# Performance work log

Hardware: AMD Instinct MI355X
Metric: run time of the kernel (lower is better)

## Reference

```python
import jax, jax.numpy as jnp
import numpy as np

B, N, C = 4, 4096, 32
S = 4096  # samples == N (square DFT matrix)


def setup_inputs() -> dict:
    key = jax.random.key(0)
    k1, k2 = jax.random.split(key)
    x = jax.random.normal(k1, (B, N, C), dtype=jnp.float32)
    t = jax.random.uniform(k2, (B, N), dtype=jnp.float32)  # sample times in [0,1]
    # learnable freqs initialized exactly as in the module: linspace(0,1,samples)
    freqs = jnp.linspace(0.0, 1.0, S).astype(jnp.float32)
    return {"x": x, "t": t, "freqs": freqs}


def reference(x, t, freqs):
    n = x.shape[1]
    # exponent_rows = -2*pi*i * (freqs*(n-1)) / n  -> purely imaginary, keep the real phase
    rows = (-2.0 * jnp.pi / n) * (freqs * (n - 1))          # [S]
    cols = t * (n - 1)                                       # [B, N]
    phase = rows[None, :, None] * cols[:, None, :]           # [B, S, N]
    fourier = jnp.exp(1j * phase.astype(jnp.complex64)) * (1.0 / np.sqrt(n)).astype(np.float32)
    z = jnp.einsum('bsn,bnc->bsc', fourier, x.astype(jnp.complex64))  # [B, S, C] complex
    # remove_zerocomp: zero first and last output rows
    z = z.at[:, 0].set(0).at[:, -1].set(0)
    # real=True -> magnitude as float32
    return jnp.abs(z).astype(jnp.float32)
```

## Files before the change

kernel.cpp:

```cpp
#include <hip/hip_runtime.h>
#include <hip/hip_fp16.h>
#include <math.h>

#define B_ 4
#define N_ 4096
#define C_ 32
#define S_ 4096
#define KW 512
#define NSTEP 16

typedef float f32x4 __attribute__((ext_vector_type(4)));
typedef _Float16 f16x8 __attribute__((ext_vector_type(8)));
typedef __fp16 fp16x2 __attribute__((ext_vector_type(2)));
typedef unsigned int uint_t;
typedef unsigned short ushort_t;

#define XTH_OFF 0
#define PSI_OFF (B_ * C_ * N_ * 2)
#define WS_NEED (PSI_OFF + B_ * N_ * 4)

__device__ __forceinline__ uint_t pkrtz(float a, float b) {
    union { fp16x2 h; uint_t w; } u;
    u.h = __builtin_amdgcn_cvt_pkrtz(a, b);
    return u.w;
}

__device__ __forceinline__ void sincos_ref(float p, float& sn, float& cs) {
    const double INV2PI_D = 0.15915494309189535;
    const float HI = (float)INV2PI_D;
    const float LO = (float)(INV2PI_D - (double)HI);
    float hi = p * HI;
    float e  = fmaf(p, HI, -hi);
    e = fmaf(p, LO, e);
    float k = rintf(hi);
    float r = (hi - k) + e;
    sn = __builtin_amdgcn_sinf(r);
    cs = __builtin_amdgcn_cosf(r);
}

__global__ __launch_bounds__(256)
void fudft_prep(const float* __restrict__ x, const float* __restrict__ t,
                ushort_t* __restrict__ xTh, float* __restrict__ psi)
{
    __shared__ ushort_t lds[64][40];
    const int tid = threadIdx.x;
    const int n0 = blockIdx.x * 64;
    const int b  = blockIdx.y;

    const float* src = x + ((size_t)b * N_ + n0) * C_;
    const int nl = tid >> 2, c0 = (tid & 3) * 8;
    const float4 v0 = *(const float4*)(src + (size_t)nl * C_ + c0);
    const float4 v1 = *(const float4*)(src + (size_t)nl * C_ + c0 + 4);
    const float vv[8] = {v0.x, v0.y, v0.z, v0.w, v1.x, v1.y, v1.z, v1.w};
    union { ushort_t u[8]; int4 i; } hp;
#pragma unroll
    for (int j = 0; j < 8; ++j) hp.u[j] = __half_as_ushort(__float2half_rn(vv[j]));
    *(int4*)&lds[nl][c0] = hp.i;

    if (tid < 64) psi[b * N_ + n0 + tid] = t[b * N_ + n0 + tid] * (float)(N_ - 1);
    __syncthreads();

    const int c = tid >> 3, oct = tid & 7;
    union { ushort_t u[8]; int4 i; } o;
#pragma unroll
    for (int j = 0; j < 8; ++j) o.u[j] = lds[oct * 8 + j][c];
    *(int4*)(xTh + ((size_t)(b * C_ + c)) * N_ + n0 + oct * 8) = o.i;
}

#define MFMA16(A, Bv, Acc) __builtin_amdgcn_mfma_f32_16x16x32_f16(A, Bv, Acc, 0, 0, 0)

__global__ __launch_bounds__(512, 4)
void fudft_mfma(const float* __restrict__ freqs,
                const ushort_t* __restrict__ xTh,
                const float* __restrict__ psi,
                float* __restrict__ out)
{
    __shared__ float red[14336];

    const int tid = threadIdx.x;
    const int wk = tid >> 6;
    const int lane = tid & 63;
    const int q = lane >> 4, r = lane & 15;
    const int b = blockIdx.y;
    const int sb = blockIdx.x * 32;

    const float rr0 = -(freqs[sb + r]      * (float)(N_ - 1)) * 0.000244140625f;
    const float rr1 = -(freqs[sb + 16 + r] * (float)(N_ - 1)) * 0.000244140625f;

    const float* pp = psi + (size_t)b * N_ + wk * KW + q * 8;
    const ushort_t* xb0 = xTh + ((size_t)(b * C_ + r)) * N_ + wk * KW + q * 8;
    const ushort_t* xb1 = xb0 + 16 * N_;

    f32x4 aRe0a = {0,0,0,0}, aIm0a = {0,0,0,0}, aRe0b = {0,0,0,0}, aIm0b = {0,0,0,0};
    f32x4 aRe1a = {0,0,0,0}, aIm1a = {0,0,0,0}, aRe1b = {0,0,0,0}, aIm1b = {0,0,0,0};

#pragma unroll
    for (int s = 0; s < NSTEP; ++s) {
        const float4 p0 = *(const float4*)(pp + s * 32);
        const float4 p1 = *(const float4*)(pp + s * 32 + 4);
        union { int4 i; f16x8 v; } b0, b1;
        b0.i = *(const int4*)(xb0 + s * 32);
        b1.i = *(const int4*)(xb1 + s * 32);

        const float ph[8] = {p0.x, p0.y, p0.z, p0.w, p1.x, p1.y, p1.z, p1.w};
        float c0v[8], s0v[8], c1v[8], s1v[8];
#pragma unroll
        for (int j = 0; j < 8; ++j) {
            float rv0 = __builtin_amdgcn_fractf(rr0 * ph[j]);
            s0v[j] = __builtin_amdgcn_sinf(rv0);
            c0v[j] = __builtin_amdgcn_cosf(rv0);
            float rv1 = __builtin_amdgcn_fractf(rr1 * ph[j]);
            s1v[j] = __builtin_amdgcn_sinf(rv1);
            c1v[j] = __builtin_amdgcn_cosf(rv1);
        }
        union { uint_t w[4]; f16x8 v; } fC0, fS0, fC1, fS1;
#pragma unroll
        for (int j = 0; j < 4; ++j) {
            fC0.w[j] = pkrtz(c0v[2*j], c0v[2*j+1]);
            fS0.w[j] = pkrtz(s0v[2*j], s0v[2*j+1]);
            fC1.w[j] = pkrtz(c1v[2*j], c1v[2*j+1]);
            fS1.w[j] = pkrtz(s1v[2*j], s1v[2*j+1]);
        }
        aRe0a = MFMA16(fC0.v, b0.v, aRe0a);  aRe0b = MFMA16(fC0.v, b1.v, aRe0b);
        aIm0a = MFMA16(fS0.v, b0.v, aIm0a);  aIm0b = MFMA16(fS0.v, b1.v, aIm0b);
        aRe1a = MFMA16(fC1.v, b0.v, aRe1a);  aRe1b = MFMA16(fC1.v, b1.v, aRe1b);
        aIm1a = MFMA16(fS1.v, b0.v, aIm1a);  aIm1b = MFMA16(fS1.v, b1.v, aIm1b);
    }

    if (wk > 0) {
        float* rb = red + (size_t)(wk - 1) * 8 * 256 + lane * 4;
        *(f32x4*)(rb + 0*256) = aRe0a;  *(f32x4*)(rb + 1*256) = aIm0a;
        *(f32x4*)(rb + 2*256) = aRe0b;  *(f32x4*)(rb + 3*256) = aIm0b;
        *(f32x4*)(rb + 4*256) = aRe1a;  *(f32x4*)(rb + 5*256) = aIm1a;
        *(f32x4*)(rb + 6*256) = aRe1b;  *(f32x4*)(rb + 7*256) = aIm1b;
    }
    __syncthreads();
    if (wk == 0) {
#pragma unroll
        for (int sl = 0; sl < 7; ++sl) {
            const float* rb = red + (size_t)sl * 8 * 256 + lane * 4;
            aRe0a += *(const f32x4*)(rb + 0*256);  aIm0a += *(const f32x4*)(rb + 1*256);
            aRe0b += *(const f32x4*)(rb + 2*256);  aIm0b += *(const f32x4*)(rb + 3*256);
            aRe1a += *(const f32x4*)(rb + 4*256);  aIm1a += *(const f32x4*)(rb + 5*256);
            aRe1b += *(const f32x4*)(rb + 6*256);  aIm1b += *(const f32x4*)(rb + 7*256);
        }
        float* po = out + ((size_t)b * S_ + sb) * C_;
#pragma unroll
        for (int reg = 0; reg < 4; ++reg) {
            const int m0 = q * 4 + reg, m1 = 16 + q * 4 + reg;
            const bool z0 = (sb + m0 == 0) || (sb + m0 == S_ - 1);
            const bool z1 = (sb + m1 == 0) || (sb + m1 == S_ - 1);
            float v;
            v = sqrtf(fmaf(aRe0a[reg], aRe0a[reg], aIm0a[reg]*aIm0a[reg])) * 0.015625f;
            po[(size_t)m0 * C_ + r]      = z0 ? 0.f : v;
            v = sqrtf(fmaf(aRe0b[reg], aRe0b[reg], aIm0b[reg]*aIm0b[reg])) * 0.015625f;
            po[(size_t)m0 * C_ + 16 + r] = z0 ? 0.f : v;
            v = sqrtf(fmaf(aRe1a[reg], aRe1a[reg], aIm1a[reg]*aIm1a[reg])) * 0.015625f;
            po[(size_t)m1 * C_ + r]      = z1 ? 0.f : v;
            v = sqrtf(fmaf(aRe1b[reg], aRe1b[reg], aIm1b[reg]*aIm1b[reg])) * 0.015625f;
            po[(size_t)m1 * C_ + 16 + r] = z1 ? 0.f : v;
        }
    }
}

__global__ __launch_bounds__(256)
void fudft_naive(const float* __restrict__ x, const float* __restrict__ t,
                 const float* __restrict__ freqs, float* __restrict__ out)
{
    const int s = blockIdx.x * 256 + threadIdx.x;
    const int b = blockIdx.y;
    const float row = (freqs[s] * (float)(N_ - 1)) * (float)(-2.0 * M_PI / (double)N_);
    float aR[C_], aI[C_];
#pragma unroll
    for (int c = 0; c < C_; ++c) { aR[c] = 0.f; aI[c] = 0.f; }
    for (int n = 0; n < N_; ++n) {
        const float col = t[b * N_ + n] * (float)(N_ - 1);
        float sn, cs; sincos_ref(row * col, sn, cs);
        const float* xr = x + ((size_t)b * N_ + n) * C_;
#pragma unroll
        for (int c = 0; c < C_; ++c) {
            aR[c] = fmaf(cs, xr[c], aR[c]);
            aI[c] = fmaf(sn, xr[c], aI[c]);
        }
    }
    float* dst = out + ((size_t)b * S_ + s) * C_;
    const bool zero = (s == 0) || (s == S_ - 1);
#pragma unroll
    for (int c = 0; c < C_; ++c) {
        const float m = sqrtf(fmaf(aR[c], aR[c], aI[c] * aI[c])) * 0.015625f;
        dst[c] = zero ? 0.f : m;
    }
}

extern "C" void kernel_launch(void* const* d_in, const int* in_sizes, int n_in,
                              void* d_out, int out_size, void* d_ws, size_t ws_size,
                              hipStream_t stream) {
    const float* x = (const float*)d_in[0];
    const float* t = (const float*)d_in[1];
    const float* f = (const float*)d_in[2];
    float* out = (float*)d_out;

    if (ws_size >= (size_t)WS_NEED) {
        char* ws = (char*)d_ws;
        ushort_t* xTh = (ushort_t*)(ws + XTH_OFF);
        float*    psi = (float*)(ws + PSI_OFF);

        dim3 gprep(N_ / 64, B_);
        fudft_prep<<<gprep, 256, 0, stream>>>(x, t, xTh, psi);
        dim3 grid(S_ / 32, B_);
        fudft_mfma<<<grid, 512, 0, stream>>>(f, xTh, psi, out);
    } else {
        dim3 grid(S_ / 256, B_);
        fudft_naive<<<grid, 256, 0, stream>>>(x, t, f, out);
    }
}
```

Measured before the change: 82.03 us.

## Split the N reduction across two blocks and add a reduce kernel

The MFMA kernel's reduction over N is split into two halves, one per grid slice. Each block writes complex partial sums to a workspace buffer, and a new reduce kernel adds the two halves and applies the magnitude and zeroing. This doubles the block count to 1024 with half the per-wave K work, targeting better occupancy and load balance. The in-block LDS reduction becomes a tree, with a smaller LDS footprint and a higher launch-bounds occupancy hint. In exchange it adds a kernel launch, an extra global round-trip of partials, and a larger workspace requirement, which could push execution onto the naive fallback if the workspace is too small.

```diff
diff --git a/kernel.cpp b/kernel.cpp
--- a/kernel.cpp
+++ b/kernel.cpp
@@ -6,8 +6,9 @@
 #define N_ 4096
 #define C_ 32
 #define S_ 4096
-#define KW 512
-#define NSTEP 16
+#define KB2 2048
+#define KW 256
+#define NSTEP 8
 
 typedef float f32x4 __attribute__((ext_vector_type(4)));
 typedef _Float16 f16x8 __attribute__((ext_vector_type(8)));
@@ -15,9 +16,11 @@
 typedef unsigned int uint_t;
 typedef unsigned short ushort_t;
 
-#define XTH_OFF 0
-#define PSI_OFF (B_ * C_ * N_ * 2)
-#define WS_NEED (PSI_OFF + B_ * N_ * 4)
+#define XTH_OFF  0
+#define PSI_OFF  (B_ * C_ * N_ * 2)
+#define PART_OFF (PSI_OFF + B_ * N_ * 4)
+#define PART_BYTES (B_ * 2 * S_ * 2 * C_ * 4)
+#define WS_NEED  (PART_OFF + PART_BYTES)
 
 __device__ __forceinline__ uint_t pkrtz(float a, float b) {
     union { fp16x2 h; uint_t w; } u;
@@ -69,26 +72,27 @@
 
 #define MFMA16(A, Bv, Acc) __builtin_amdgcn_mfma_f32_16x16x32_f16(A, Bv, Acc, 0, 0, 0)
 
-__global__ __launch_bounds__(512, 4)
+__global__ __launch_bounds__(512, 8)
 void fudft_mfma(const float* __restrict__ freqs,
                 const ushort_t* __restrict__ xTh,
                 const float* __restrict__ psi,
-                float* __restrict__ out)
-{
-    __shared__ float red[14336];
+                float* __restrict__ part)
+{
+    __shared__ float red[8192];
 
     const int tid = threadIdx.x;
     const int wk = tid >> 6;
     const int lane = tid & 63;
     const int q = lane >> 4, r = lane & 15;
-    const int b = blockIdx.y;
+    const int kh = blockIdx.y;
+    const int b = blockIdx.z;
     const int sb = blockIdx.x * 32;
 
     const float rr0 = -(freqs[sb + r]      * (float)(N_ - 1)) * 0.000244140625f;
     const float rr1 = -(freqs[sb + 16 + r] * (float)(N_ - 1)) * 0.000244140625f;
 
-    const float* pp = psi + (size_t)b * N_ + wk * KW + q * 8;
-    const ushort_t* xb0 = xTh + ((size_t)(b * C_ + r)) * N_ + wk * KW + q * 8;
+    const float* pp = psi + (size_t)b * N_ + kh * KB2 + wk * KW + q * 8;
+    const ushort_t* xb0 = xTh + ((size_t)(b * C_ + r)) * N_ + kh * KB2 + wk * KW + q * 8;
     const ushort_t* xb1 = xb0 + 16 * N_;
 
     f32x4 aRe0a = {0,0,0,0}, aIm0a = {0,0,0,0}, aRe0b = {0,0,0,0}, aIm0b = {0,0,0,0};
@@ -127,40 +131,60 @@
         aIm1a = MFMA16(fS1.v, b0.v, aIm1a);  aIm1b = MFMA16(fS1.v, b1.v, aIm1b);
     }
 
-    if (wk > 0) {
-        float* rb = red + (size_t)(wk - 1) * 8 * 256 + lane * 4;
+    auto store_slot = [&](int slot) {
+        float* rb = red + slot * 2048 + lane * 4;
         *(f32x4*)(rb + 0*256) = aRe0a;  *(f32x4*)(rb + 1*256) = aIm0a;
         *(f32x4*)(rb + 2*256) = aRe0b;  *(f32x4*)(rb + 3*256) = aIm0b;
         *(f32x4*)(rb + 4*256) = aRe1a;  *(f32x4*)(rb + 5*256) = aIm1a;
         *(f32x4*)(rb + 6*256) = aRe1b;  *(f32x4*)(rb + 7*256) = aIm1b;
-    }
+    };
+    auto add_slot = [&](int slot) {
+        const float* rb = red + slot * 2048 + lane * 4;
+        aRe0a += *(const f32x4*)(rb + 0*256);  aIm0a += *(const f32x4*)(rb + 1*256);
+        aRe0b += *(const f32x4*)(rb + 2*256);  aIm0b += *(const f32x4*)(rb + 3*256);
+        aRe1a += *(const f32x4*)(rb + 4*256);  aIm1a += *(const f32x4*)(rb + 5*256);
+        aRe1b += *(const f32x4*)(rb + 6*256);  aIm1b += *(const f32x4*)(rb + 7*256);
+    };
+
+    if (wk >= 4) store_slot(wk - 4);
+    __syncthreads();
+    if (wk < 4) add_slot(wk);
+    __syncthreads();
+    if (wk == 2 || wk == 3) store_slot(wk - 2);
+    __syncthreads();
+    if (wk < 2) add_slot(wk);
+    __syncthreads();
+    if (wk == 1) store_slot(0);
     __syncthreads();
     if (wk == 0) {
-#pragma unroll
-        for (int sl = 0; sl < 7; ++sl) {
-            const float* rb = red + (size_t)sl * 8 * 256 + lane * 4;
-            aRe0a += *(const f32x4*)(rb + 0*256);  aIm0a += *(const f32x4*)(rb + 1*256);
-            aRe0b += *(const f32x4*)(rb + 2*256);  aIm0b += *(const f32x4*)(rb + 3*256);
-            aRe1a += *(const f32x4*)(rb + 4*256);  aIm1a += *(const f32x4*)(rb + 5*256);
-            aRe1b += *(const f32x4*)(rb + 6*256);  aIm1b += *(const f32x4*)(rb + 7*256);
-        }
-        float* po = out + ((size_t)b * S_ + sb) * C_;
+        add_slot(0);
+        float* po = part + (((size_t)(b * 2 + kh) * S_ + sb) * C_) * 2;
 #pragma unroll
         for (int reg = 0; reg < 4; ++reg) {
             const int m0 = q * 4 + reg, m1 = 16 + q * 4 + reg;
-            const bool z0 = (sb + m0 == 0) || (sb + m0 == S_ - 1);
-            const bool z1 = (sb + m1 == 0) || (sb + m1 == S_ - 1);
-            float v;
-            v = sqrtf(fmaf(aRe0a[reg], aRe0a[reg], aIm0a[reg]*aIm0a[reg])) * 0.015625f;
-            po[(size_t)m0 * C_ + r]      = z0 ? 0.f : v;
-            v = sqrtf(fmaf(aRe0b[reg], aRe0b[reg], aIm0b[reg]*aIm0b[reg])) * 0.015625f;
-            po[(size_t)m0 * C_ + 16 + r] = z0 ? 0.f : v;
-            v = sqrtf(fmaf(aRe1a[reg], aRe1a[reg], aIm1a[reg]*aIm1a[reg])) * 0.015625f;
-            po[(size_t)m1 * C_ + r]      = z1 ? 0.f : v;
-            v = sqrtf(fmaf(aRe1b[reg], aRe1b[reg], aIm1b[reg]*aIm1b[reg])) * 0.015625f;
-            po[(size_t)m1 * C_ + 16 + r] = z1 ? 0.f : v;
-        }
-    }
+            *(float2*)(po + ((size_t)m0 * C_ + r) * 2)      = make_float2(aRe0a[reg], aIm0a[reg]);
+            *(float2*)(po + ((size_t)m0 * C_ + 16 + r) * 2) = make_float2(aRe0b[reg], aIm0b[reg]);
+            *(float2*)(po + ((size_t)m1 * C_ + r) * 2)      = make_float2(aRe1a[reg], aIm1a[reg]);
+            *(float2*)(po + ((size_t)m1 * C_ + 16 + r) * 2) = make_float2(aRe1b[reg], aIm1b[reg]);
+        }
+    }
+}
+
+__global__ __launch_bounds__(256)
+void fudft_reduce(const float* __restrict__ part, float* __restrict__ out)
+{
+    const int idx = blockIdx.x * 256 + threadIdx.x;
+    const int c2 = (idx & 15) * 2;
+    const int s = (idx >> 4) & (S_ - 1);
+    const int b = idx >> 16;
+    const float4 v0 = *(const float4*)(part + (((size_t)(b * 2 + 0) * S_ + s) * C_ + c2) * 2);
+    const float4 v1 = *(const float4*)(part + (((size_t)(b * 2 + 1) * S_ + s) * C_ + c2) * 2);
+    const float re0 = v0.x + v1.x, im0 = v0.y + v1.y;
+    const float re1 = v0.z + v1.z, im1 = v0.w + v1.w;
+    float m0 = sqrtf(fmaf(re0, re0, im0 * im0)) * 0.015625f;
+    float m1 = sqrtf(fmaf(re1, re1, im1 * im1)) * 0.015625f;
+    if (s == 0 || s == S_ - 1) { m0 = 0.f; m1 = 0.f; }
+    *(float2*)(out + ((size_t)b * S_ + s) * C_ + c2) = make_float2(m0, m1);
 }
 
 __global__ __launch_bounds__(256)
@@ -202,13 +226,15 @@
 
     if (ws_size >= (size_t)WS_NEED) {
         char* ws = (char*)d_ws;
-        ushort_t* xTh = (ushort_t*)(ws + XTH_OFF);
-        float*    psi = (float*)(ws + PSI_OFF);
+        ushort_t* xTh  = (ushort_t*)(ws + XTH_OFF);
+        float*    psi  = (float*)(ws + PSI_OFF);
+        float*    part = (float*)(ws + PART_OFF);
 
         dim3 gprep(N_ / 64, B_);
         fudft_prep<<<gprep, 256, 0, stream>>>(x, t, xTh, psi);
-        dim3 grid(S_ / 32, B_);
-        fudft_mfma<<<grid, 512, 0, stream>>>(f, xTh, psi, out);
+        dim3 grid(S_ / 32, 2, B_);
+        fudft_mfma<<<grid, 512, 0, stream>>>(f, xTh, psi, part);
+        fudft_reduce<<<(B_ * S_ * C_ / 2) / 256, 256, 0, stream>>>(part, out);
     } else {
         dim3 grid(S_ / 256, B_);
         fudft_naive<<<grid, 256, 0, stream>>>(x, t, f, out);
```

New measurement: 109.5 us. 33.5% more time.
